# Optimization experiments

Hardware: AMD Instinct MI355X
Metric: run time of the kernel (lower is better)

## Reference

```python
import jax, jax.numpy as jnp
import numpy as np

DIM = 512
HEADS = 8
HD = DIM // HEADS

def _rotate_half(t):
    t1, t2 = jnp.split(t, 2, axis=-1)
    return jnp.concatenate((-t2, t1), axis=-1)

def _layernorm(x, g, b, eps=1e-5):
    mu = jnp.mean(x, axis=-1, keepdims=True)
    var = jnp.var(x, axis=-1, keepdims=True)
    return (x - mu) * jax.lax.rsqrt(var + eps) * g + b

def setup_inputs() -> dict:
    key = jax.random.key(0)
    ks = jax.random.split(key, 12)
    B, S = 4, 2048
    x = jax.random.normal(ks[0], (B, S, DIM), dtype=jnp.float32)
    rope_cos = jax.random.uniform(ks[1], (1, S, 1, HD), dtype=jnp.float32)
    rope_sin = jax.random.uniform(ks[2], (1, S, 1, HD), dtype=jnp.float32)
    sd = 1.0 / np.sqrt(DIM)
    params = {
        'norm1_g': jnp.ones((DIM,), jnp.float32),
        'norm1_b': jnp.zeros((DIM,), jnp.float32),
        'norm2_g': jnp.ones((DIM,), jnp.float32),
        'norm2_b': jnp.zeros((DIM,), jnp.float32),
        'w_qkv': jax.random.uniform(ks[3], (DIM, 3 * DIM), jnp.float32, -sd, sd),
        'b_qkv': jax.random.uniform(ks[4], (3 * DIM,), jnp.float32, -sd, sd),
        'w_proj': jax.random.uniform(ks[5], (DIM, DIM), jnp.float32, -sd, sd),
        'b_proj': jax.random.uniform(ks[6], (DIM,), jnp.float32, -sd, sd),
        'w_fc1': jax.random.uniform(ks[7], (DIM, 4 * DIM), jnp.float32, -sd, sd),
        'b_fc1': jax.random.uniform(ks[8], (4 * DIM,), jnp.float32, -sd, sd),
        'w_fc2': jax.random.uniform(ks[9], (4 * DIM, DIM), jnp.float32, -1.0 / np.sqrt(4 * DIM), 1.0 / np.sqrt(4 * DIM)),
        'b_fc2': jax.random.uniform(ks[10], (DIM,), jnp.float32, -1.0 / np.sqrt(4 * DIM), 1.0 / np.sqrt(4 * DIM)),
    }
    return {'x': x, 'rope_cos': rope_cos, 'rope_sin': rope_sin, **params}

def reference(x, rope_cos, rope_sin, norm1_g, norm1_b, norm2_g, norm2_b,
              w_qkv, b_qkv, w_proj, b_proj, w_fc1, b_fc1, w_fc2, b_fc2):
    B, S, D = x.shape
    scale = 1.0 / np.sqrt(HD)
    shortcut = x
    h = _layernorm(x, norm1_g, norm1_b)
    qkv = (h @ w_qkv + b_qkv).reshape(B, S, 3, HEADS, HD)
    q, k, v = qkv[:, :, 0], qkv[:, :, 1], qkv[:, :, 2]  # [B,S,H,hd]
    q = q * rope_cos + _rotate_half(q) * rope_sin
    k = k * rope_cos + _rotate_half(k) * rope_sin
    # attention over heads: scores [B,H,S,S]
    attn = jnp.einsum('bqhd,bkhd->bhqk', q, k) * scale
    attn = jax.nn.softmax(attn, axis=-1)
    o = jnp.einsum('bhqk,bkhd->bqhd', attn, v).reshape(B, S, D)
    o = o @ w_proj + b_proj
    x = shortcut + o  # dropout is identity in eval
    h2 = _layernorm(x, norm2_g, norm2_b)
    mlp = jax.nn.gelu(h2 @ w_fc1 + b_fc1, approximate=False) @ w_fc2 + b_fc2
    return x + mlp
```

## Files before the change

kernel.cpp:

```cpp
#include <hip/hip_runtime.h>
#include <cstdint>
#include <cstddef>

typedef unsigned short u16;
typedef unsigned int   u32;
typedef __bf16 bf16x8 __attribute__((ext_vector_type(8)));
typedef float  f32x4  __attribute__((ext_vector_type(4)));

#define BS   8192
#define DIMM 512
#define NH   8
#define HD   64
#define SEQ  2048
#define DFF  2048
#define NQKV 1536

#define GLD16(g, l) __builtin_amdgcn_global_load_lds( \
    (__attribute__((address_space(1))) const void*)(g), \
    (__attribute__((address_space(3))) void*)(l), 16, 0, 0)

__device__ __forceinline__ float b2f(u16 s) {
  u32 u = ((u32)s) << 16;
  float f; __builtin_memcpy(&f, &u, 4); return f;
}
__device__ __forceinline__ u16 f2b(float f) {
  u32 u; __builtin_memcpy(&u, &f, 4);
  u += 0x7fffu + ((u >> 16) & 1u);
  return (u16)(u >> 16);
}
__device__ __forceinline__ u16 f2b_rtz(float f) {
  u32 u; __builtin_memcpy(&u, &f, 4);
  return (u16)(u >> 16);
}

#define SZ_QKV (DIMM * NQKV)
#define SZ_PRJ (DIMM * DIMM)
#define SZ_F1  (DIMM * DFF)
#define SZ_F2  (DFF * DIMM)
__global__ __launch_bounds__(256) void transpose_all_k(
    const float* __restrict__ w_qkv, const float* __restrict__ w_prj,
    const float* __restrict__ w_f1,  const float* __restrict__ w_f2,
    u16* __restrict__ o_qkv, u16* __restrict__ o_prj,
    u16* __restrict__ o_f1,  u16* __restrict__ o_f2) {
  int idx = blockIdx.x * 256 + threadIdx.x;
  const float* W; u16* O; int Kd, Nd, off;
  if (idx < SZ_QKV)                         { W = w_qkv; O = o_qkv; Kd = DIMM; Nd = NQKV; off = idx; }
  else if (idx < SZ_QKV + SZ_PRJ)           { W = w_prj; O = o_prj; Kd = DIMM; Nd = DIMM; off = idx - SZ_QKV; }
  else if (idx < SZ_QKV + SZ_PRJ + SZ_F1)   { W = w_f1;  O = o_f1;  Kd = DIMM; Nd = DFF;  off = idx - SZ_QKV - SZ_PRJ; }
  else                                      { W = w_f2;  O = o_f2;  Kd = DFF;  Nd = DIMM; off = idx - SZ_QKV - SZ_PRJ - SZ_F1; }
  int n = off / Kd, k = off - n * Kd;
  O[off] = f2b(W[(size_t)k * Nd + n]);
}

__global__ __launch_bounds__(256) void ln_f32b_k(const float* __restrict__ X,
    const float* __restrict__ G, const float* __restrict__ Bb, u16* __restrict__ out) {
  int w = threadIdx.x >> 6, lane = threadIdx.x & 63;
  size_t row = (size_t)blockIdx.x * 4 + w;
  const float* xr = X + row * DIMM;
  float v[8];
  *(float4*)&v[0] = *(const float4*)(xr + lane * 8);
  *(float4*)&v[4] = *(const float4*)(xr + lane * 8 + 4);
  float s = 0.f, s2 = 0.f;
#pragma unroll
  for (int j = 0; j < 8; j++) { s += v[j]; s2 += v[j] * v[j]; }
#pragma unroll
  for (int m = 1; m < 64; m <<= 1) { s += __shfl_xor(s, m); s2 += __shfl_xor(s2, m); }
  float mu = s * (1.f / DIMM);
  float rsd = rsqrtf(s2 * (1.f / DIMM) - mu * mu + 1e-5f);
  float g[8], bb[8];
  *(float4*)&g[0]  = *(const float4*)(G + lane * 8);
  *(float4*)&g[4]  = *(const float4*)(G + lane * 8 + 4);
  *(float4*)&bb[0] = *(const float4*)(Bb + lane * 8);
  *(float4*)&bb[4] = *(const float4*)(Bb + lane * 8 + 4);
  uint4 ov; u16* os = (u16*)&ov;
#pragma unroll
  for (int j = 0; j < 8; j++) os[j] = f2b((v[j] - mu) * rsd * g[j] + bb[j]);
  *(uint4*)(out + row * DIMM + lane * 8) = ov;
}

template <int EPI, int TM>
__global__ __launch_bounds__(256) void gemm_bt(const u16* __restrict__ A,
    const u16* __restrict__ BT, const float* __restrict__ bias,
    void* __restrict__ Cout, const float* __restrict__ resid, int N, int Kd) {
  __shared__ u16 a_s[TM * 32];
  __shared__ u16 b_s[128 * 32];
  int t = threadIdx.x, lane = t & 63, w = t >> 6;
  int l15 = lane & 15, quad = lane >> 4;
  int gx = gridDim.x;
  int lid = blockIdx.x + gx * blockIdx.y;
  int per = (gx * gridDim.y) >> 3;
  int nid = (lid & 7) * per + (lid >> 3);
  int bx = nid % gx, by = nid / gx;
  int m0 = by * TM, n0 = bx * 128;
  constexpr int MT = TM / 32;
  int wm = (w >> 1) * (TM / 2), wn = (w & 1) * 64;
  f32x4 z4 = {0.f, 0.f, 0.f, 0.f};
  f32x4 acc[MT][4];
#pragma unroll
  for (int i = 0; i < MT; i++)
#pragma unroll
    for (int j = 0; j < 4; j++) acc[i][j] = z4;

  for (int k0 = 0; k0 < Kd; k0 += 32) {
    __syncthreads();
#pragma unroll
    for (int i = 0; i < TM / 64; i++) {
      int c = t + i * 256;
      int row = c >> 2, ch = c & 3;
      GLD16(A + (size_t)(m0 + row) * Kd + k0 + ch * 8, &a_s[c * 8]);
    }
#pragma unroll
    for (int i = 0; i < 2; i++) {
      int c = t + i * 256;
      int row = c >> 2, ch = c & 3;
      GLD16(BT + (size_t)(n0 + row) * Kd + k0 + ch * 8, &b_s[c * 8]);
    }
    __syncthreads();
    bf16x8 af[MT], bfm[4];
#pragma unroll
    for (int mt = 0; mt < MT; mt++) af[mt] = *(const bf16x8*)&a_s[(wm + mt * 16 + l15) * 32 + quad * 8];
#pragma unroll
    for (int nt = 0; nt < 4; nt++) bfm[nt] = *(const bf16x8*)&b_s[(wn + nt * 16 + l15) * 32 + quad * 8];
#pragma unroll
    for (int mt = 0; mt < MT; mt++)
#pragma unroll
      for (int nt = 0; nt < 4; nt++)
        acc[mt][nt] = __builtin_amdgcn_mfma_f32_16x16x32_bf16(af[mt], bfm[nt], acc[mt][nt], 0, 0, 0);
  }

#pragma unroll
  for (int nt = 0; nt < 4; nt++) {
    int col = n0 + wn + nt * 16 + l15;
    float bv = bias[col];
#pragma unroll
    for (int mt = 0; mt < MT; mt++) {
#pragma unroll
      for (int r = 0; r < 4; r++) {
        int rw = m0 + wm + mt * 16 + quad * 4 + r;
        float v = acc[mt][nt][r] + bv;
        size_t off = (size_t)rw * N + col;
        if (EPI == 0) {
          ((float*)Cout)[off] = v;
        } else if (EPI == 1) {
          ((float*)Cout)[off] = v + resid[off];
        } else if (EPI == 2) {
          ((u16*)Cout)[off] = f2b(0.5f * v * (1.f + erff(v * 0.70710678118654752f)));
        } else {
          ((u16*)Cout)[off] = f2b(v);
        }
      }
    }
  }
}

#define QSCALE 0.18033688f
__global__ __launch_bounds__(256) void rope_k(const u16* __restrict__ qkv,
    const float* __restrict__ C, const float* __restrict__ Sn,
    u16* __restrict__ Qo, u16* __restrict__ Ko, u16* __restrict__ Vo) {
  int idx = blockIdx.x * 256 + threadIdx.x;
  int row = idx / 192;
  int cn = idx - row * 192;
  int n0 = cn * 8;
  int comp = n0 >> 9;
  int hh = (n0 >> 6) & 7;
  int d0 = n0 & 63;
  int b = row >> 11, s = row & 2047;
  const u16* src = qkv + (size_t)row * NQKV;
  uint4 val = *(const uint4*)(src + n0);
  u16* vs = (u16*)&val;
  size_t oo = ((size_t)((b << 3) + hh) * SEQ + s) * HD + d0;
  if (comp == 2) { *(uint4*)(Vo + oo) = val; return; }
  uint4 pv = *(const uint4*)(src + (n0 ^ 32));
  u16* ps = (u16*)&pv;
  float cv[8], sv[8];
  *(float4*)&cv[0] = *(const float4*)(C + s * HD + d0);
  *(float4*)&cv[4] = *(const float4*)(C + s * HD + d0 + 4);
  *(float4*)&sv[0] = *(const float4*)(Sn + s * HD + d0);
  *(float4*)&sv[4] = *(const float4*)(Sn + s * HD + d0 + 4);
  float sgn = (d0 & 32) ? 1.f : -1.f;
  float sc = (comp == 0) ? QSCALE : 1.f;
  uint4 ov; u16* os = (u16*)&ov;
#pragma unroll
  for (int j = 0; j < 8; j++)
    os[j] = f2b(sc * (b2f(vs[j]) * cv[j] + sgn * b2f(ps[j]) * sv[j]));
  *(uint4*)((comp == 0 ? Qo : Ko) + oo) = ov;
}

__global__ __launch_bounds__(256) void attn_flash_k(const u16* __restrict__ Qg,
    const u16* __restrict__ Kg, const u16* __restrict__ Vg, u16* __restrict__ Og) {
  __shared__ u16 q_s[128 * 72];
  __shared__ u16 k_s[64 * 72];
  __shared__ u16 vt_s[64 * 72];
  int t = threadIdx.x, lane = t & 63, w = t >> 6;
  int l15 = lane & 15, quad = lane >> 4;
  int lid = blockIdx.x;
  int nid = (lid & 7) * 64 + (lid >> 3);
  int bh = nid >> 4;
  int qt0 = (nid & 15) * 128;
  int b = bh >> 3, h = bh & 7;
  const u16* Qp = Qg + (size_t)bh * SEQ * HD;
  const u16* Kp = Kg + (size_t)bh * SEQ * HD;
  const u16* Vp = Vg + (size_t)bh * SEQ * HD;
  int row0 = t >> 3, ch = t & 7;
  int row1 = row0 + 32;
  int r8a = row0 >> 3, r0a = row0 & 7;
  int r8b = row1 >> 3, r0b = row1 & 7;

#pragma unroll
  for (int i = 0; i < 4; i++) {
    int c = t + i * 256, qr = c >> 3, qc = c & 7;
    *(uint4*)&q_s[qr * 72 + qc * 8] = *(const uint4*)(Qp + (size_t)(qt0 + qr) * HD + qc * 8);
  }
  uint4 kr0 = *(const uint4*)(Kp + (size_t)row0 * HD + ch * 8);
  uint4 kr1 = *(const uint4*)(Kp + (size_t)row1 * HD + ch * 8);
  uint4 vr0 = *(const uint4*)(Vp + (size_t)row0 * HD + ch * 8);
  uint4 vr1 = *(const uint4*)(Vp + (size_t)row1 * HD + ch * 8);
  __syncthreads();
  bf16x8 qa[2][2];
#pragma unroll
  for (int rs = 0; rs < 2; rs++) {
    qa[rs][0] = *(const bf16x8*)&q_s[(rs * 64 + w * 16 + l15) * 72 + quad * 8];
    qa[rs][1] = *(const bf16x8*)&q_s[(rs * 64 + w * 16 + l15) * 72 + 32 + quad * 8];
  }
  u16* p_s = q_s;
  f32x4 z4 = {0.f, 0.f, 0.f, 0.f};
  f32x4 of[2][4];
#pragma unroll
  for (int rs = 0; rs < 2; rs++)
#pragma unroll
    for (int n = 0; n < 4; n++) of[rs][n] = z4;
  float lrun[2][4] = {};

  for (int kt = 0; kt < SEQ; kt += 64) {
    __syncthreads();
    *(uint4*)&k_s[row0 * 72 + ch * 8] = kr0;
    *(uint4*)&k_s[row1 * 72 + ch * 8] = kr1;
    {
      u16* v0 = (u16*)&vr0; u16* v1 = (u16*)&vr1;
#pragma unroll
      for (int j = 0; j < 8; j++) {
        int d = ch * 8 + j;
        vt_s[d * 72 + ((r8a ^ ch) << 3) + r0a] = v0[j];
        vt_s[d * 72 + ((r8b ^ ch) << 3) + r0b] = v1[j];
      }
    }
    __syncthreads();
    if (kt + 64 < SEQ) {
      kr0 = *(const uint4*)(Kp + (size_t)(kt + 64 + row0) * HD + ch * 8);
      kr1 = *(const uint4*)(Kp + (size_t)(kt + 64 + row1) * HD + ch * 8);
      vr0 = *(const uint4*)(Vp + (size_t)(kt + 64 + row0) * HD + ch * 8);
      vr1 = *(const uint4*)(Vp + (size_t)(kt + 64 + row1) * HD + ch * 8);
    }
    f32x4 sf[2][4];
#pragma unroll
    for (int rs = 0; rs < 2; rs++)
#pragma unroll
      for (int n = 0; n < 4; n++) sf[rs][n] = z4;
#pragma unroll
    for (int kk = 0; kk < 2; kk++)
#pragma unroll
      for (int n = 0; n < 4; n++) {
        bf16x8 kb = *(const bf16x8*)&k_s[(n * 16 + l15) * 72 + kk * 32 + quad * 8];
        sf[0][n] = __builtin_amdgcn_mfma_f32_16x16x32_bf16(qa[0][kk], kb, sf[0][n], 0, 0, 0);
        sf[1][n] = __builtin_amdgcn_mfma_f32_16x16x32_bf16(qa[1][kk], kb, sf[1][n], 0, 0, 0);
      }
#pragma unroll
    for (int rs = 0; rs < 2; rs++)
#pragma unroll
      for (int r = 0; r < 4; r++) {
        int prow = (rs * 64 + w * 16 + quad * 4 + r) * 72;
#pragma unroll
        for (int n = 0; n < 4; n++) {
          float pp = exp2f(sf[rs][n][r]);
          lrun[rs][r] += pp;
          p_s[prow + n * 16 + l15] = f2b_rtz(pp);
        }
      }
#pragma unroll
    for (int kk = 0; kk < 2; kk++) {
      bf16x8 pa0 = *(const bf16x8*)&p_s[(w * 16 + l15) * 72 + kk * 32 + quad * 8];
      bf16x8 pa1 = *(const bf16x8*)&p_s[(64 + w * 16 + l15) * 72 + kk * 32 + quad * 8];
#pragma unroll
      for (int n = 0; n < 4; n++) {
        bf16x8 vb = *(const bf16x8*)&vt_s[(n * 16 + l15) * 72 +
                     (((kk * 4 + quad) ^ (2 * n + (l15 >> 3))) << 3)];
        of[0][n] = __builtin_amdgcn_mfma_f32_16x16x32_bf16(pa0, vb, of[0][n], 0, 0, 0);
        of[1][n] = __builtin_amdgcn_mfma_f32_16x16x32_bf16(pa1, vb, of[1][n], 0, 0, 0);
      }
    }
  }
#pragma unroll
  for (int rs = 0; rs < 2; rs++)
#pragma unroll
    for (int r = 0; r < 4; r++) {
      float l = lrun[rs][r];
#pragma unroll
      for (int m = 1; m < 16; m <<= 1) l += __shfl_xor(l, m);
      float inv = 1.f / l;
      size_t orow = (size_t)(b * SEQ + qt0 + rs * 64 + w * 16 + quad * 4 + r);
#pragma unroll
      for (int n = 0; n < 4; n++)
        Og[orow * DIMM + h * HD + n * 16 + l15] = f2b(of[rs][n][r] * inv);
    }
}

extern "C" void kernel_launch(void* const* d_in, const int* in_sizes, int n_in,
                              void* d_out, int out_size, void* d_ws, size_t ws_size,
                              hipStream_t stream) {
  const float* x    = (const float*)d_in[0];
  const float* rc   = (const float*)d_in[1];
  const float* rsn  = (const float*)d_in[2];
  const float* n1g  = (const float*)d_in[3];
  const float* n1b  = (const float*)d_in[4];
  const float* n2g  = (const float*)d_in[5];
  const float* n2b  = (const float*)d_in[6];
  const float* wqkv = (const float*)d_in[7];
  const float* bqkv = (const float*)d_in[8];
  const float* wprj = (const float*)d_in[9];
  const float* bprj = (const float*)d_in[10];
  const float* wf1  = (const float*)d_in[11];
  const float* bf1  = (const float*)d_in[12];
  const float* wf2  = (const float*)d_in[13];
  const float* bf2  = (const float*)d_in[14];

  char* p = (char*)d_ws;
  u16*   wqkvT = (u16*)p;
  u16*   wprjT = (u16*)(p + (2u  << 20));
  u16*   wf1T  = (u16*)(p + (3u  << 20));
  u16*   wf2T  = (u16*)(p + (5u  << 20));
  u16*   h1    = (u16*)(p + (8u  << 20));
  u16*   qkvb  = (u16*)(p + (16u << 20));
  u16*   Qb    = (u16*)(p + (64u << 20));
  u16*   Kb    = (u16*)(p + (72u << 20));
  u16*   Vb    = (u16*)(p + (80u << 20));
  float* x2    = (float*)(p + (88u << 20));
  u16*   ob    = h1;
  u16*   h2    = h1;
  u16*   mid   = qkvb;

  transpose_all_k<<<dim3((SZ_QKV + SZ_PRJ + SZ_F1 + SZ_F2) / 256), 256, 0, stream>>>(
      wqkv, wprj, wf1, wf2, wqkvT, wprjT, wf1T, wf2T);

  ln_f32b_k<<<dim3(BS / 4), 256, 0, stream>>>(x, n1g, n1b, h1);

  gemm_bt<3, 128><<<dim3(NQKV / 128, BS / 128), 256, 0, stream>>>(h1, wqkvT, bqkv, qkvb, nullptr, NQKV, DIMM);

  rope_k<<<dim3(BS * NQKV / 8 / 256), 256, 0, stream>>>(qkvb, rc, rsn, Qb, Kb, Vb);

  attn_flash_k<<<dim3(32 * (SEQ / 128)), 256, 0, stream>>>(Qb, Kb, Vb, ob);

  gemm_bt<1, 64><<<dim3(DIMM / 128, BS / 64), 256, 0, stream>>>(ob, wprjT, bprj, x2, x, DIMM, DIMM);

  ln_f32b_k<<<dim3(BS / 4), 256, 0, stream>>>(x2, n2g, n2b, h2);

  gemm_bt<2, 128><<<dim3(DFF / 128, BS / 128), 256, 0, stream>>>(h2, wf1T, bf1, mid, nullptr, DFF, DIMM);

  gemm_bt<1, 64><<<dim3(DIMM / 128, BS / 64), 256, 0, stream>>>(mid, wf2T, bf2, (float*)d_out, x2, DIMM, DFF);
}
```

Baseline: 318.1 us.

## Split attention query tile across 8 waves and add MFMA priority hints

The flash attention block now runs 512 threads (8 waves) instead of 256. Each wave handles 16 query rows instead of 32, and each thread loads a single K/V row per tile. s_setprio is raised around the MFMA sections so waves in their matrix phase get issue priority over waves in their exp phase. This halves per-thread registers and adds more waves to hide latency. The cost is less reuse of each K/V fragment per wave and barriers shared across more waves.

```diff
diff --git a/kernel.cpp b/kernel.cpp
--- a/kernel.cpp
+++ b/kernel.cpp
@@ -186,7 +186,7 @@
   *(uint4*)((comp == 0 ? Qo : Ko) + oo) = ov;
 }
 
-__global__ __launch_bounds__(256) void attn_flash_k(const u16* __restrict__ Qg,
+__global__ __launch_bounds__(512) void attn_flash_k(const u16* __restrict__ Qg,
     const u16* __restrict__ Kg, const u16* __restrict__ Vg, u16* __restrict__ Og) {
   __shared__ u16 q_s[128 * 72];
   __shared__ u16 k_s[64 * 72];
@@ -201,107 +201,89 @@
   const u16* Qp = Qg + (size_t)bh * SEQ * HD;
   const u16* Kp = Kg + (size_t)bh * SEQ * HD;
   const u16* Vp = Vg + (size_t)bh * SEQ * HD;
-  int row0 = t >> 3, ch = t & 7;
-  int row1 = row0 + 32;
-  int r8a = row0 >> 3, r0a = row0 & 7;
-  int r8b = row1 >> 3, r0b = row1 & 7;
-
-#pragma unroll
-  for (int i = 0; i < 4; i++) {
-    int c = t + i * 256, qr = c >> 3, qc = c & 7;
+  int row = t >> 3, ch = t & 7;
+  int r8 = row >> 3, r0 = row & 7;
+
+#pragma unroll
+  for (int i = 0; i < 2; i++) {
+    int c = t + i * 512, qr = c >> 3, qc = c & 7;
     *(uint4*)&q_s[qr * 72 + qc * 8] = *(const uint4*)(Qp + (size_t)(qt0 + qr) * HD + qc * 8);
   }
-  uint4 kr0 = *(const uint4*)(Kp + (size_t)row0 * HD + ch * 8);
-  uint4 kr1 = *(const uint4*)(Kp + (size_t)row1 * HD + ch * 8);
-  uint4 vr0 = *(const uint4*)(Vp + (size_t)row0 * HD + ch * 8);
-  uint4 vr1 = *(const uint4*)(Vp + (size_t)row1 * HD + ch * 8);
+  uint4 kr = *(const uint4*)(Kp + (size_t)row * HD + ch * 8);
+  uint4 vr = *(const uint4*)(Vp + (size_t)row * HD + ch * 8);
   __syncthreads();
-  bf16x8 qa[2][2];
-#pragma unroll
-  for (int rs = 0; rs < 2; rs++) {
-    qa[rs][0] = *(const bf16x8*)&q_s[(rs * 64 + w * 16 + l15) * 72 + quad * 8];
-    qa[rs][1] = *(const bf16x8*)&q_s[(rs * 64 + w * 16 + l15) * 72 + 32 + quad * 8];
-  }
+  bf16x8 qa[2];
+  qa[0] = *(const bf16x8*)&q_s[(w * 16 + l15) * 72 + quad * 8];
+  qa[1] = *(const bf16x8*)&q_s[(w * 16 + l15) * 72 + 32 + quad * 8];
   u16* p_s = q_s;
   f32x4 z4 = {0.f, 0.f, 0.f, 0.f};
-  f32x4 of[2][4];
-#pragma unroll
-  for (int rs = 0; rs < 2; rs++)
-#pragma unroll
-    for (int n = 0; n < 4; n++) of[rs][n] = z4;
-  float lrun[2][4] = {};
+  f32x4 of[4];
+#pragma unroll
+  for (int n = 0; n < 4; n++) of[n] = z4;
+  float lrun[4] = {};
 
   for (int kt = 0; kt < SEQ; kt += 64) {
     __syncthreads();
-    *(uint4*)&k_s[row0 * 72 + ch * 8] = kr0;
-    *(uint4*)&k_s[row1 * 72 + ch * 8] = kr1;
+    *(uint4*)&k_s[row * 72 + ch * 8] = kr;
     {
-      u16* v0 = (u16*)&vr0; u16* v1 = (u16*)&vr1;
+      u16* v0 = (u16*)&vr;
 #pragma unroll
       for (int j = 0; j < 8; j++) {
         int d = ch * 8 + j;
-        vt_s[d * 72 + ((r8a ^ ch) << 3) + r0a] = v0[j];
-        vt_s[d * 72 + ((r8b ^ ch) << 3) + r0b] = v1[j];
+        vt_s[d * 72 + ((r8 ^ ch) << 3) + r0] = v0[j];
       }
     }
     __syncthreads();
     if (kt + 64 < SEQ) {
-      kr0 = *(const uint4*)(Kp + (size_t)(kt + 64 + row0) * HD + ch * 8);
-      kr1 = *(const uint4*)(Kp + (size_t)(kt + 64 + row1) * HD + ch * 8);
-      vr0 = *(const uint4*)(Vp + (size_t)(kt + 64 + row0) * HD + ch * 8);
-      vr1 = *(const uint4*)(Vp + (size_t)(kt + 64 + row1) * HD + ch * 8);
-    }
-    f32x4 sf[2][4];
-#pragma unroll
-    for (int rs = 0; rs < 2; rs++)
-#pragma unroll
-      for (int n = 0; n < 4; n++) sf[rs][n] = z4;
+      kr = *(const uint4*)(Kp + (size_t)(kt + 64 + row) * HD + ch * 8);
+      vr = *(const uint4*)(Vp + (size_t)(kt + 64 + row) * HD + ch * 8);
+    }
+    f32x4 sf[4];
+#pragma unroll
+    for (int n = 0; n < 4; n++) sf[n] = z4;
+    __builtin_amdgcn_s_setprio(1);
 #pragma unroll
     for (int kk = 0; kk < 2; kk++)
 #pragma unroll
       for (int n = 0; n < 4; n++) {
         bf16x8 kb = *(const bf16x8*)&k_s[(n * 16 + l15) * 72 + kk * 32 + quad * 8];
-        sf[0][n] = __builtin_amdgcn_mfma_f32_16x16x32_bf16(qa[0][kk], kb, sf[0][n], 0, 0, 0);
-        sf[1][n] = __builtin_amdgcn_mfma_f32_16x16x32_bf16(qa[1][kk], kb, sf[1][n], 0, 0, 0);
-      }
-#pragma unroll
-    for (int rs = 0; rs < 2; rs++)
-#pragma unroll
-      for (int r = 0; r < 4; r++) {
-        int prow = (rs * 64 + w * 16 + quad * 4 + r) * 72;
-#pragma unroll
-        for (int n = 0; n < 4; n++) {
-          float pp = exp2f(sf[rs][n][r]);
-          lrun[rs][r] += pp;
-          p_s[prow + n * 16 + l15] = f2b_rtz(pp);
-        }
-      }
+        sf[n] = __builtin_amdgcn_mfma_f32_16x16x32_bf16(qa[kk], kb, sf[n], 0, 0, 0);
+      }
+    __builtin_amdgcn_s_setprio(0);
+#pragma unroll
+    for (int r = 0; r < 4; r++) {
+      int prow = (w * 16 + quad * 4 + r) * 72;
+#pragma unroll
+      for (int n = 0; n < 4; n++) {
+        float pp = exp2f(sf[n][r]);
+        lrun[r] += pp;
+        p_s[prow + n * 16 + l15] = f2b_rtz(pp);
+      }
+    }
+    __builtin_amdgcn_s_setprio(1);
 #pragma unroll
     for (int kk = 0; kk < 2; kk++) {
-      bf16x8 pa0 = *(const bf16x8*)&p_s[(w * 16 + l15) * 72 + kk * 32 + quad * 8];
-      bf16x8 pa1 = *(const bf16x8*)&p_s[(64 + w * 16 + l15) * 72 + kk * 32 + quad * 8];
+      bf16x8 pa = *(const bf16x8*)&p_s[(w * 16 + l15) * 72 + kk * 32 + quad * 8];
 #pragma unroll
       for (int n = 0; n < 4; n++) {
         bf16x8 vb = *(const bf16x8*)&vt_s[(n * 16 + l15) * 72 +
                      (((kk * 4 + quad) ^ (2 * n + (l15 >> 3))) << 3)];
-        of[0][n] = __builtin_amdgcn_mfma_f32_16x16x32_bf16(pa0, vb, of[0][n], 0, 0, 0);
-        of[1][n] = __builtin_amdgcn_mfma_f32_16x16x32_bf16(pa1, vb, of[1][n], 0, 0, 0);
-      }
-    }
-  }
-#pragma unroll
-  for (int rs = 0; rs < 2; rs++)
-#pragma unroll
-    for (int r = 0; r < 4; r++) {
-      float l = lrun[rs][r];
-#pragma unroll
-      for (int m = 1; m < 16; m <<= 1) l += __shfl_xor(l, m);
-      float inv = 1.f / l;
-      size_t orow = (size_t)(b * SEQ + qt0 + rs * 64 + w * 16 + quad * 4 + r);
-#pragma unroll
-      for (int n = 0; n < 4; n++)
-        Og[orow * DIMM + h * HD + n * 16 + l15] = f2b(of[rs][n][r] * inv);
-    }
+        of[n] = __builtin_amdgcn_mfma_f32_16x16x32_bf16(pa, vb, of[n], 0, 0, 0);
+      }
+    }
+    __builtin_amdgcn_s_setprio(0);
+  }
+#pragma unroll
+  for (int r = 0; r < 4; r++) {
+    float l = lrun[r];
+#pragma unroll
+    for (int m = 1; m < 16; m <<= 1) l += __shfl_xor(l, m);
+    float inv = 1.f / l;
+    size_t orow = (size_t)(b * SEQ + qt0 + w * 16 + quad * 4 + r);
+#pragma unroll
+    for (int n = 0; n < 4; n++)
+      Og[orow * DIMM + h * HD + n * 16 + l15] = f2b(of[n][r] * inv);
+  }
 }
 
 extern "C" void kernel_launch(void* const* d_in, const int* in_sizes, int n_in,
@@ -347,7 +329,7 @@
 
   rope_k<<<dim3(BS * NQKV / 8 / 256), 256, 0, stream>>>(qkvb, rc, rsn, Qb, Kb, Vb);
 
-  attn_flash_k<<<dim3(32 * (SEQ / 128)), 256, 0, stream>>>(Qb, Kb, Vb, ob);
+  attn_flash_k<<<dim3(32 * (SEQ / 128)), 512, 0, stream>>>(Qb, Kb, Vb, ob);
 
   gemm_bt<1, 64><<<dim3(DIMM / 128, BS / 64), 256, 0, stream>>>(ob, wprjT, bprj, x2, x, DIMM, DIMM);
 
```

Measured after the change: 312.5 us. Within noise of the previous version (-1.8%).
